# Performance work log

Hardware: AMD Instinct MI355X
Metric: run time of the kernel (lower is better)

## Reference

```python
import jax, jax.numpy as jnp
import numpy as np

N_NODES = 100000
N_EDGES = 3200000
IN_CH, HID, OUT_CH = 602, 16, 41


def setup_inputs() -> dict:
    key = jax.random.key(0)
    ks = jax.random.split(key, 5)
    x = jax.random.normal(ks[0], (N_NODES, IN_CH), dtype=jnp.float32)
    edge_index = jax.random.randint(ks[1], (2, N_EDGES), 0, N_NODES, dtype=jnp.int32)
    # glorot init for weights, zeros for biases (matches reset_parameters)
    W1 = jax.random.normal(ks[2], (IN_CH, HID), dtype=jnp.float32) * np.sqrt(2.0 / (IN_CH + HID))
    b1 = jnp.zeros((HID,), dtype=jnp.float32)
    W2 = jax.random.normal(ks[3], (HID, OUT_CH), dtype=jnp.float32) * np.sqrt(2.0 / (HID + OUT_CH))
    b2 = jnp.zeros((OUT_CH,), dtype=jnp.float32)
    return {"x": x, "edge_index": edge_index, "W1": W1, "b1": b1, "W2": W2, "b2": b2}


def _sage_conv(x, src, dst, W, b, n_nodes):
    # linear transform first (16-wide), then gather-scatter-mean over edges
    h = x @ W                                   # [N, out]
    msg = h[src]                                # [E, out] gather of source nodes
    agg = jax.ops.segment_sum(msg, dst, num_segments=n_nodes)          # [N, out]
    cnt = jax.ops.segment_sum(jnp.ones((src.shape[0], 1), h.dtype), dst,
                              num_segments=n_nodes)                     # [N, 1]
    mean = agg / jnp.maximum(cnt, 1.0)          # scatter-mean (0 for isolated nodes)
    return mean + b


def reference(x, edge_index, W1, b1, W2, b2):
    src, dst = edge_index[0], edge_index[1]     # source_to_target flow
    n = x.shape[0]
    h = jax.nn.relu(_sage_conv(x, src, dst, W1, b1, n))
    # F.dropout(training=False) -> identity (inference mode)
    out = _sage_conv(h, src, dst, W2, b2, n)
    return jax.nn.log_softmax(out, axis=1)
```

## Files before the change

### kernel.cpp

```cpp
#include <hip/hip_runtime.h>
#include <hip/hip_fp16.h>
#include <cmath>

#define NN 100000
#define NE 3200000
#define CIN 602
#define CH 16
#define COUT 41
#define TB 128
#define KTL 32
#define KSPLIT 4

#define NPB 128
#define NB  ((NN + NPB - 1) / NPB)
#define EPC 32
#define ECHUNK (256 * EPC)
#define EB  ((NE + ECHUNK - 1) / ECHUNK)

__device__ float  g_part[KSPLIT * NN * CH];
__device__ __half g_h1h[NN * CH];
__device__ __half g_h1bh[NN * CH];
__device__ int   g_rs[NN + 1];
__device__ int   g_csr[NE];
__device__ int2  g_pair[NE];
__device__ int   g_cnt[NB * EB];
__device__ int   g_colsum[NB];
__device__ int   g_bbase[NB + 1];

__device__ __forceinline__ int clamp_node(int v) {
    return v < 0 ? 0 : (v >= NN ? NN - 1 : v);
}

__global__ __launch_bounds__(256) void fallback_zero_out_k(float* __restrict__ out, int n) {
    int i = blockIdx.x * blockDim.x + threadIdx.x;
    if (i < n) out[i] = 0.0f;
}

__global__ __launch_bounds__(256) void count_k(const int* __restrict__ ei) {
    __shared__ int h[NB];
    const int t = threadIdx.x;
    for (int i = t; i < NB; i += 256) h[i] = 0;
    __syncthreads();
    const int base = blockIdx.x * ECHUNK;
#pragma unroll
    for (int j = 0; j < EPC; ++j) {
        int e = base + j * 256 + t;
        if (e < NE) {
            int d = clamp_node(ei[NE + e]);
            atomicAdd(&h[d >> 7], 1);
        }
    }
    __syncthreads();
    for (int i = t; i < NB; i += 256) g_cnt[i * EB + blockIdx.x] = h[i];
}

__global__ __launch_bounds__(256) void scanA_k() {
    const int b = blockIdx.x;
    const int t = threadIdx.x;
    __shared__ int a[512];
    __shared__ int sh[256];
    a[t]       = (t < EB)       ? g_cnt[b * EB + t]       : 0;
    a[t + 256] = (t + 256 < EB) ? g_cnt[b * EB + t + 256] : 0;
    __syncthreads();
    int e0 = a[2 * t], e1 = a[2 * t + 1];
    int sum = e0 + e1;
    sh[t] = sum;
    __syncthreads();
    for (int off = 1; off < 256; off <<= 1) {
        int v = (t >= off) ? sh[t - off] : 0;
        __syncthreads();
        sh[t] += v;
        __syncthreads();
    }
    int run = sh[t] - sum;
    if (2 * t < EB)     g_cnt[b * EB + 2 * t]     = run;
    if (2 * t + 1 < EB) g_cnt[b * EB + 2 * t + 1] = run + e0;
    if (t == 255) g_colsum[b] = sh[255];
}

__global__ __launch_bounds__(1024) void scanB_k() {
    const int t = threadIdx.x;
    __shared__ int sh[1024];
    int v = (t < NB) ? g_colsum[t] : 0;
    sh[t] = v;
    __syncthreads();
    for (int off = 1; off < 1024; off <<= 1) {
        int u = (t >= off) ? sh[t - off] : 0;
        __syncthreads();
        sh[t] += u;
        __syncthreads();
    }
    if (t < NB) g_bbase[t] = sh[t] - v;
    if (t == 1023) {
        g_bbase[NB] = sh[1023];
        g_rs[NN]    = sh[1023];
    }
}

__global__ __launch_bounds__(256) void scatter_k(const int* __restrict__ ei) {
    __shared__ int lb[NB];
    const int t = threadIdx.x;
    for (int i = t; i < NB; i += 256)
        lb[i] = g_bbase[i] + g_cnt[i * EB + blockIdx.x];
    __syncthreads();
    const int base = blockIdx.x * ECHUNK;
#pragma unroll
    for (int j = 0; j < EPC; ++j) {
        int e = base + j * 256 + t;
        if (e < NE) {
            int s = clamp_node(ei[e]);
            int d = clamp_node(ei[NE + e]);
            int p = atomicAdd(&lb[d >> 7], 1);
            g_pair[p] = make_int2(s, d);
        }
    }
}

__global__ __launch_bounds__(256) void build_k() {
    const int b = blockIdx.x;
    const int t = threadIdx.x;
    const int n0 = b * NPB;
    const int e0 = g_bbase[b], e1 = g_bbase[b + 1];
    __shared__ int ldeg[NPB];
    __shared__ int lrs[NPB + 1];
    __shared__ int lcur[NPB];
    if (t < NPB) ldeg[t] = 0;
    __syncthreads();
    for (int e = e0 + t; e < e1; e += 256) {
        int2 p = g_pair[e];
        atomicAdd(&ldeg[p.y - n0], 1);
    }
    __syncthreads();
    if (t == 0) {
        int run = 0;
        for (int i = 0; i < NPB; ++i) { lrs[i] = run; run += ldeg[i]; }
        lrs[NPB] = run;
    }
    __syncthreads();
    if (t < NPB) {
        int node = n0 + t;
        if (node < NN) g_rs[node] = e0 + lrs[t];
        lcur[t] = lrs[t];
    }
    __syncthreads();
    for (int e = e0 + t; e < e1; e += 256) {
        int2 p = g_pair[e];
        int r = atomicAdd(&lcur[p.y - n0], 1);
        g_csr[e0 + r] = p.x;
    }
}

__global__ __launch_bounds__(TB) void gemm1_k(const float* __restrict__ x,
                                              const float* __restrict__ W1) {
    __shared__ float xs[KTL][TB + 1];
    const int bid = blockIdx.x;
    const int h   = bid & 3;
    const int rblk = bid >> 2;
    const int t = threadIdx.x;
    const int l  = t & 15;
    const int rg = t >> 4;
    const int row0 = rblk * TB;
    const int row  = row0 + t;
    const int kbase = h * 160;
    const int NT = (h < 3) ? 5 : 4;

    float acc[CH];
#pragma unroll
    for (int c = 0; c < CH; ++c) acc[c] = 0.f;

    float2 ld[16];

    auto stage_load = [&](int ti) {
        const int kb = kbase + KTL * ti;
        const bool colok = (h < 3) || (ti < 3) || (l <= 12);
#pragma unroll
        for (int p = 0; p < 16; ++p) {
            int rgl = row0 + rg + 8 * p;
            ld[p] = (rgl < NN && colok)
                ? *reinterpret_cast<const float2*>(x + (size_t)rgl * CIN + kb + 2 * l)
                : make_float2(0.f, 0.f);
        }
    };
    auto stage_store = [&]() {
#pragma unroll
        for (int p = 0; p < 16; ++p) {
            int rl = rg + 8 * p;
            xs[2 * l][rl]     = ld[p].x;
            xs[2 * l + 1][rl] = ld[p].y;
        }
    };
    auto fma_col = [&](int krow, float xv) {
        const float4* w4 = reinterpret_cast<const float4*>(W1 + (size_t)krow * CH);
        float4 w0 = w4[0], w1 = w4[1], w2 = w4[2], w3 = w4[3];
        acc[0]  += xv * w0.x; acc[1]  += xv * w0.y; acc[2]  += xv * w0.z; acc[3]  += xv * w0.w;
        acc[4]  += xv * w1.x; acc[5]  += xv * w1.y; acc[6]  += xv * w1.z; acc[7]  += xv * w1.w;
        acc[8]  += xv * w2.x; acc[9]  += xv * w2.y; acc[10] += xv * w2.z; acc[11] += xv * w2.w;
        acc[12] += xv * w3.x; acc[13] += xv * w3.y; acc[14] += xv * w3.z; acc[15] += xv * w3.w;
    };

    stage_load(0);
    for (int ti = 0; ti < NT; ++ti) {
        stage_store();
        __syncthreads();
        if (ti < NT - 1) stage_load(ti + 1);
        const int kb = kbase + KTL * ti;
        if (h < 3 || ti < 3) {
#pragma unroll 8
            for (int kk = 0; kk < KTL; ++kk) fma_col(kb + kk, xs[kk][t]);
        } else {
#pragma unroll 13
            for (int kk = 0; kk < 26; ++kk) fma_col(kb + kk, xs[kk][t]);
        }
        __syncthreads();
    }

    if (row < NN) {
        float4* pp = reinterpret_cast<float4*>(g_part + ((size_t)h * NN + row) * CH);
        pp[0] = make_float4(acc[0],  acc[1],  acc[2],  acc[3]);
        pp[1] = make_float4(acc[4],  acc[5],  acc[6],  acc[7]);
        pp[2] = make_float4(acc[8],  acc[9],  acc[10], acc[11]);
        pp[3] = make_float4(acc[12], acc[13], acc[14], acc[15]);
    }
}

__global__ __launch_bounds__(256) void combine_k() {
    int node = blockIdx.x * blockDim.x + threadIdx.x;
    if (node >= NN) return;
    float s[CH];
#pragma unroll
    for (int h = 0; h < KSPLIT; ++h) {
        const float4* pp = reinterpret_cast<const float4*>(g_part + ((size_t)h * NN + node) * CH);
        float4 p0 = pp[0], p1 = pp[1], p2 = pp[2], p3 = pp[3];
        if (h == 0) {
            s[0]=p0.x; s[1]=p0.y; s[2]=p0.z; s[3]=p0.w;
            s[4]=p1.x; s[5]=p1.y; s[6]=p1.z; s[7]=p1.w;
            s[8]=p2.x; s[9]=p2.y; s[10]=p2.z; s[11]=p2.w;
            s[12]=p3.x; s[13]=p3.y; s[14]=p3.z; s[15]=p3.w;
        } else {
            s[0]+=p0.x; s[1]+=p0.y; s[2]+=p0.z; s[3]+=p0.w;
            s[4]+=p1.x; s[5]+=p1.y; s[6]+=p1.z; s[7]+=p1.w;
            s[8]+=p2.x; s[9]+=p2.y; s[10]+=p2.z; s[11]+=p2.w;
            s[12]+=p3.x; s[13]+=p3.y; s[14]+=p3.z; s[15]+=p3.w;
        }
    }
    __half2 pk[8];
#pragma unroll
    for (int c = 0; c < 8; ++c)
        pk[c] = __float22half2_rn(make_float2(s[2 * c], s[2 * c + 1]));
    uint4* hp = reinterpret_cast<uint4*>(&g_h1h[(size_t)node * CH]);
    hp[0] = *reinterpret_cast<uint4*>(&pk[0]);
    hp[1] = *reinterpret_cast<uint4*>(&pk[4]);
}

__global__ __launch_bounds__(256) void gather1_k(const float* __restrict__ b1) {
    int gtid = blockIdx.x * blockDim.x + threadIdx.x;
    int node = gtid >> 6;
    int l    = gtid & 63;
    int q    = l & 3;
    int es   = l >> 2;
    int start = g_rs[node], end = g_rs[node + 1];
    float4 acc = make_float4(0.f, 0.f, 0.f, 0.f);
    int e = start + es;
    for (; e + 16 < end; e += 32) {
        int s0 = g_csr[e], s1 = g_csr[e + 16];
        uint2 ua = *reinterpret_cast<const uint2*>(&g_h1h[(size_t)s0 * CH + (q << 2)]);
        uint2 ub = *reinterpret_cast<const uint2*>(&g_h1h[(size_t)s1 * CH + (q << 2)]);
        float2 fa0 = __half22float2(*reinterpret_cast<__half2*>(&ua.x));
        float2 fa1 = __half22float2(*reinterpret_cast<__half2*>(&ua.y));
        float2 fb0 = __half22float2(*reinterpret_cast<__half2*>(&ub.x));
        float2 fb1 = __half22float2(*reinterpret_cast<__half2*>(&ub.y));
        acc.x += fa0.x + fb0.x; acc.y += fa0.y + fb0.y;
        acc.z += fa1.x + fb1.x; acc.w += fa1.y + fb1.y;
    }
    if (e < end) {
        int s0 = g_csr[e];
        uint2 ua = *reinterpret_cast<const uint2*>(&g_h1h[(size_t)s0 * CH + (q << 2)]);
        float2 fa0 = __half22float2(*reinterpret_cast<__half2*>(&ua.x));
        float2 fa1 = __half22float2(*reinterpret_cast<__half2*>(&ua.y));
        acc.x += fa0.x; acc.y += fa0.y; acc.z += fa1.x; acc.w += fa1.y;
    }
#pragma unroll
    for (int off = 4; off < 64; off <<= 1) {
        acc.x += __shfl_xor(acc.x, off, 64);
        acc.y += __shfl_xor(acc.y, off, 64);
        acc.z += __shfl_xor(acc.z, off, 64);
        acc.w += __shfl_xor(acc.w, off, 64);
    }
    if (l < 4) {
        float inv = 1.0f / fmaxf((float)(end - start), 1.0f);
        float4 bv = reinterpret_cast<const float4*>(b1)[l];
        __half2 h0 = __float22half2_rn(make_float2(fmaxf(acc.x * inv + bv.x, 0.f),
                                                   fmaxf(acc.y * inv + bv.y, 0.f)));
        __half2 h1 = __float22half2_rn(make_float2(fmaxf(acc.z * inv + bv.z, 0.f),
                                                   fmaxf(acc.w * inv + bv.w, 0.f)));
        uint2 u;
        u.x = *reinterpret_cast<unsigned*>(&h0);
        u.y = *reinterpret_cast<unsigned*>(&h1);
        *reinterpret_cast<uint2*>(&g_h1bh[(size_t)node * CH + (l << 2)]) = u;
    }
}

__global__ __launch_bounds__(256) void g2final_k(const float* __restrict__ W2,
                                                 const float* __restrict__ b2,
                                                 float* __restrict__ out) {
    __shared__ float w2s[CH * COUT];
    const int t = threadIdx.x;
    for (int i = t; i < CH * COUT; i += 256) w2s[i] = W2[i];
    __syncthreads();

    int gtid = blockIdx.x * blockDim.x + t;
    int node = gtid >> 6;
    int l    = gtid & 63;
    int q    = l & 3;
    int es   = l >> 2;
    int start = g_rs[node], end = g_rs[node + 1];
    float4 acc = make_float4(0.f, 0.f, 0.f, 0.f);
    int e = start + es;
    for (; e + 16 < end; e += 32) {
        int s0 = g_csr[e], s1 = g_csr[e + 16];
        uint2 ua = *reinterpret_cast<const uint2*>(&g_h1bh[(size_t)s0 * CH + (q << 2)]);
        uint2 ub = *reinterpret_cast<const uint2*>(&g_h1bh[(size_t)s1 * CH + (q << 2)]);
        float2 fa0 = __half22float2(*reinterpret_cast<__half2*>(&ua.x));
        float2 fa1 = __half22float2(*reinterpret_cast<__half2*>(&ua.y));
        float2 fb0 = __half22float2(*reinterpret_cast<__half2*>(&ub.x));
        float2 fb1 = __half22float2(*reinterpret_cast<__half2*>(&ub.y));
        acc.x += fa0.x + fb0.x; acc.y += fa0.y + fb0.y;
        acc.z += fa1.x + fb1.x; acc.w += fa1.y + fb1.y;
    }
    if (e < end) {
        int s0 = g_csr[e];
        uint2 ua = *reinterpret_cast<const uint2*>(&g_h1bh[(size_t)s0 * CH + (q << 2)]);
        float2 fa0 = __half22float2(*reinterpret_cast<__half2*>(&ua.x));
        float2 fa1 = __half22float2(*reinterpret_cast<__half2*>(&ua.y));
        acc.x += fa0.x; acc.y += fa0.y; acc.z += fa1.x; acc.w += fa1.y;
    }
#pragma unroll
    for (int off = 4; off < 64; off <<= 1) {
        acc.x += __shfl_xor(acc.x, off, 64);
        acc.y += __shfl_xor(acc.y, off, 64);
        acc.z += __shfl_xor(acc.z, off, 64);
        acc.w += __shfl_xor(acc.w, off, 64);
    }
    float a16[CH];
#pragma unroll
    for (int k = 0; k < CH; ++k) {
        float comp = ((k & 3) == 0) ? acc.x : ((k & 3) == 1) ? acc.y
                   : ((k & 3) == 2) ? acc.z : acc.w;
        a16[k] = __shfl(comp, k >> 2, 64);
    }
    float inv = 1.0f / fmaxf((float)(end - start), 1.0f);
    float o = -INFINITY;
    if (l < COUT) {
        float s = 0.f;
#pragma unroll
        for (int k = 0; k < CH; ++k) s += a16[k] * w2s[k * COUT + l];
        o = s * inv + b2[l];
    }
    float m = o;
#pragma unroll
    for (int off = 32; off > 0; off >>= 1) m = fmaxf(m, __shfl_xor(m, off, 64));
    float ex = (l < COUT) ? expf(o - m) : 0.0f;
    float ssum = ex;
#pragma unroll
    for (int off = 32; off > 0; off >>= 1) ssum += __shfl_xor(ssum, off, 64);
    if (l < COUT) out[(size_t)node * COUT + l] = o - m - logf(ssum);
}

extern "C" void kernel_launch(void* const* d_in, const int* in_sizes, int n_in,
                              void* d_out, int out_size, void* d_ws, size_t ws_size,
                              hipStream_t stream) {
    (void)d_ws; (void)ws_size;
    float* out = (float*)d_out;

    const int expect[6] = {NN * CIN, 2 * NE, CIN * CH, CH, CH * COUT, COUT};
    bool ok = (n_in >= 6) && (out_size == NN * COUT);
    if (ok) {
        for (int i = 0; i < 6; ++i)
            if (in_sizes[i] != expect[i]) { ok = false; break; }
    }
    if (!ok) {
        int n = out_size > 0 ? out_size : 1;
        fallback_zero_out_k<<<(n + 255) / 256, 256, 0, stream>>>(out, n);
        return;
    }

    const float* x  = (const float*)d_in[0];
    const int*   ei = (const int*)d_in[1];
    const float* W1 = (const float*)d_in[2];
    const float* b1 = (const float*)d_in[3];
    const float* W2 = (const float*)d_in[4];
    const float* b2 = (const float*)d_in[5];

    const int WAVE_BLKS = (NN * 64 + 255) / 256;
    const int G1_BLKS   = ((NN + TB - 1) / TB) * KSPLIT;

    count_k  <<<EB, 256, 0, stream>>>(ei);
    scanA_k  <<<NB, 256, 0, stream>>>();
    scanB_k  <<<1, 1024, 0, stream>>>();
    scatter_k<<<EB, 256, 0, stream>>>(ei);
    build_k  <<<NB, 256, 0, stream>>>();
    gemm1_k  <<<G1_BLKS, TB, 0, stream>>>(x, W1);
    combine_k<<<(NN + 255) / 256, 256, 0, stream>>>();
    gather1_k<<<WAVE_BLKS, 256, 0, stream>>>(b1);
    g2final_k<<<WAVE_BLKS, 256, 0, stream>>>(W2, b2, out);
}
```

Baseline: 597.1 us.

## Pack edge pairs into 32-bit words and use nontemporal loads/stores

```diff
diff --git a/kernel.cpp b/kernel.cpp
--- a/kernel.cpp
+++ b/kernel.cpp
@@ -17,18 +17,22 @@
 #define ECHUNK (256 * EPC)
 #define EB  ((NE + ECHUNK - 1) / ECHUNK)
 
-__device__ float  g_part[KSPLIT * NN * CH];
-__device__ __half g_h1h[NN * CH];
-__device__ __half g_h1bh[NN * CH];
-__device__ int   g_rs[NN + 1];
-__device__ int   g_csr[NE];
-__device__ int2  g_pair[NE];
-__device__ int   g_cnt[NB * EB];
-__device__ int   g_colsum[NB];
-__device__ int   g_bbase[NB + 1];
+__device__ float    g_part[KSPLIT * NN * CH];
+__device__ __half   g_h1h[NN * CH];
+__device__ __half   g_h1bh[NN * CH];
+__device__ int      g_rs[NN + 1];
+__device__ int      g_csr[NE];
+__device__ unsigned g_pack[NE];
+__device__ int      g_cnt[NB * EB];
+__device__ int      g_colsum[NB];
+__device__ int      g_bbase[NB + 1];
 
 __device__ __forceinline__ int clamp_node(int v) {
     return v < 0 ? 0 : (v >= NN ? NN - 1 : v);
+}
+__device__ __forceinline__ float2 nt_load_f2(const float* p) {
+    double d = __builtin_nontemporal_load(reinterpret_cast<const double*>(p));
+    return *reinterpret_cast<float2*>(&d);
 }
 
 __global__ __launch_bounds__(256) void fallback_zero_out_k(float* __restrict__ out, int n) {
@@ -46,7 +50,7 @@
     for (int j = 0; j < EPC; ++j) {
         int e = base + j * 256 + t;
         if (e < NE) {
-            int d = clamp_node(ei[NE + e]);
+            int d = clamp_node(__builtin_nontemporal_load(&ei[NE + e]));
             atomicAdd(&h[d >> 7], 1);
         }
     }
@@ -108,10 +112,11 @@
     for (int j = 0; j < EPC; ++j) {
         int e = base + j * 256 + t;
         if (e < NE) {
-            int s = clamp_node(ei[e]);
-            int d = clamp_node(ei[NE + e]);
+            int s = clamp_node(__builtin_nontemporal_load(&ei[e]));
+            int d = clamp_node(__builtin_nontemporal_load(&ei[NE + e]));
             int p = atomicAdd(&lb[d >> 7], 1);
-            g_pair[p] = make_int2(s, d);
+            unsigned v = (unsigned)s | ((unsigned)(d & 127) << 17);
+            __builtin_nontemporal_store(v, &g_pack[p]);
         }
     }
 }
@@ -127,8 +132,8 @@
     if (t < NPB) ldeg[t] = 0;
     __syncthreads();
     for (int e = e0 + t; e < e1; e += 256) {
-        int2 p = g_pair[e];
-        atomicAdd(&ldeg[p.y - n0], 1);
+        unsigned v = __builtin_nontemporal_load(&g_pack[e]);
+        atomicAdd(&ldeg[v >> 17], 1);
     }
     __syncthreads();
     if (t == 0) {
@@ -144,9 +149,9 @@
     }
     __syncthreads();
     for (int e = e0 + t; e < e1; e += 256) {
-        int2 p = g_pair[e];
-        int r = atomicAdd(&lcur[p.y - n0], 1);
-        g_csr[e0 + r] = p.x;
+        unsigned v = __builtin_nontemporal_load(&g_pack[e]);
+        int r = atomicAdd(&lcur[v >> 17], 1);
+        __builtin_nontemporal_store((int)(v & 0x1FFFF), &g_csr[e0 + r]);
     }
 }
 
@@ -177,7 +182,7 @@
         for (int p = 0; p < 16; ++p) {
             int rgl = row0 + rg + 8 * p;
             ld[p] = (rgl < NN && colok)
-                ? *reinterpret_cast<const float2*>(x + (size_t)rgl * CIN + kb + 2 * l)
+                ? nt_load_f2(x + (size_t)rgl * CIN + kb + 2 * l)
                 : make_float2(0.f, 0.f);
         }
     };
@@ -215,11 +220,13 @@
     }
 
     if (row < NN) {
-        float4* pp = reinterpret_cast<float4*>(g_part + ((size_t)h * NN + row) * CH);
-        pp[0] = make_float4(acc[0],  acc[1],  acc[2],  acc[3]);
-        pp[1] = make_float4(acc[4],  acc[5],  acc[6],  acc[7]);
-        pp[2] = make_float4(acc[8],  acc[9],  acc[10], acc[11]);
-        pp[3] = make_float4(acc[12], acc[13], acc[14], acc[15]);
+        float* pp = g_part + ((size_t)h * NN + row) * CH;
+#pragma unroll
+        for (int c = 0; c < CH; c += 2) {
+            double d;
+            *reinterpret_cast<float2*>(&d) = make_float2(acc[c], acc[c + 1]);
+            __builtin_nontemporal_store(d, reinterpret_cast<double*>(pp + c));
+        }
     }
 }
 
@@ -247,9 +254,10 @@
 #pragma unroll
     for (int c = 0; c < 8; ++c)
         pk[c] = __float22half2_rn(make_float2(s[2 * c], s[2 * c + 1]));
-    uint4* hp = reinterpret_cast<uint4*>(&g_h1h[(size_t)node * CH]);
-    hp[0] = *reinterpret_cast<uint4*>(&pk[0]);
-    hp[1] = *reinterpret_cast<uint4*>(&pk[4]);
+    double* hp = reinterpret_cast<double*>(&g_h1h[(size_t)node * CH]);
+#pragma unroll
+    for (int w = 0; w < 4; ++w)
+        __builtin_nontemporal_store(reinterpret_cast<const double*>(pk)[w], hp + w);
 }
 
 __global__ __launch_bounds__(256) void gather1_k(const float* __restrict__ b1) {
@@ -262,7 +270,8 @@
     float4 acc = make_float4(0.f, 0.f, 0.f, 0.f);
     int e = start + es;
     for (; e + 16 < end; e += 32) {
-        int s0 = g_csr[e], s1 = g_csr[e + 16];
+        int s0 = __builtin_nontemporal_load(&g_csr[e]);
+        int s1 = __builtin_nontemporal_load(&g_csr[e + 16]);
         uint2 ua = *reinterpret_cast<const uint2*>(&g_h1h[(size_t)s0 * CH + (q << 2)]);
         uint2 ub = *reinterpret_cast<const uint2*>(&g_h1h[(size_t)s1 * CH + (q << 2)]);
         float2 fa0 = __half22float2(*reinterpret_cast<__half2*>(&ua.x));
@@ -273,7 +282,7 @@
         acc.z += fa1.x + fb1.x; acc.w += fa1.y + fb1.y;
     }
     if (e < end) {
-        int s0 = g_csr[e];
+        int s0 = __builtin_nontemporal_load(&g_csr[e]);
         uint2 ua = *reinterpret_cast<const uint2*>(&g_h1h[(size_t)s0 * CH + (q << 2)]);
         float2 fa0 = __half22float2(*reinterpret_cast<__half2*>(&ua.x));
         float2 fa1 = __half22float2(*reinterpret_cast<__half2*>(&ua.y));
@@ -293,10 +302,11 @@
                                                    fmaxf(acc.y * inv + bv.y, 0.f)));
         __half2 h1 = __float22half2_rn(make_float2(fmaxf(acc.z * inv + bv.z, 0.f),
                                                    fmaxf(acc.w * inv + bv.w, 0.f)));
-        uint2 u;
-        u.x = *reinterpret_cast<unsigned*>(&h0);
-        u.y = *reinterpret_cast<unsigned*>(&h1);
-        *reinterpret_cast<uint2*>(&g_h1bh[(size_t)node * CH + (l << 2)]) = u;
+        double d;
+        reinterpret_cast<unsigned*>(&d)[0] = *reinterpret_cast<unsigned*>(&h0);
+        reinterpret_cast<unsigned*>(&d)[1] = *reinterpret_cast<unsigned*>(&h1);
+        __builtin_nontemporal_store(d,
+            reinterpret_cast<double*>(&g_h1bh[(size_t)node * CH + (l << 2)]));
     }
 }
 
@@ -317,7 +327,8 @@
     float4 acc = make_float4(0.f, 0.f, 0.f, 0.f);
     int e = start + es;
     for (; e + 16 < end; e += 32) {
-        int s0 = g_csr[e], s1 = g_csr[e + 16];
+        int s0 = __builtin_nontemporal_load(&g_csr[e]);
+        int s1 = __builtin_nontemporal_load(&g_csr[e + 16]);
         uint2 ua = *reinterpret_cast<const uint2*>(&g_h1bh[(size_t)s0 * CH + (q << 2)]);
         uint2 ub = *reinterpret_cast<const uint2*>(&g_h1bh[(size_t)s1 * CH + (q << 2)]);
         float2 fa0 = __half22float2(*reinterpret_cast<__half2*>(&ua.x));
@@ -328,7 +339,7 @@
         acc.z += fa1.x + fb1.x; acc.w += fa1.y + fb1.y;
     }
     if (e < end) {
-        int s0 = g_csr[e];
+        int s0 = __builtin_nontemporal_load(&g_csr[e]);
         uint2 ua = *reinterpret_cast<const uint2*>(&g_h1bh[(size_t)s0 * CH + (q << 2)]);
         float2 fa0 = __half22float2(*reinterpret_cast<__half2*>(&ua.x));
         float2 fa1 = __half22float2(*reinterpret_cast<__half2*>(&ua.y));
@@ -363,7 +374,8 @@
     float ssum = ex;
 #pragma unroll
     for (int off = 32; off > 0; off >>= 1) ssum += __shfl_xor(ssum, off, 64);
-    if (l < COUT) out[(size_t)node * COUT + l] = o - m - logf(ssum);
+    if (l < COUT)
+        __builtin_nontemporal_store(o - m - logf(ssum), &out[(size_t)node * COUT + l]);
 }
 
 extern "C" void kernel_launch(void* const* d_in, const int* in_sizes, int n_in,
```

Measured after the change: 762.3 us. 27.7% more time.
